# Kernel tuning notes

Measured on AMD Instinct MI355X. Metric: run time of the kernel, lower is better.

## Reference

```python
import jax, jax.numpy as jnp
import numpy as np

B, T, D, M, L = 4, 2048, 256, 128, 16
P = M * L  # max_pair_cnt


def setup_inputs() -> dict:
    key = jax.random.key(0)
    ks = jax.random.split(key, 11)
    head = jax.random.normal(ks[0], (B, P, T), jnp.float32) * 0.05
    tail = jax.random.normal(ks[1], (B, P, T), jnp.float32) * 0.05
    x = jax.random.normal(ks[2], (B, T, D), jnp.float32)
    coref_mention_position = jax.random.uniform(ks[3], (B, M, T), jnp.float32)
    lab = jax.random.uniform(ks[4], (B, P, 2), jnp.float32) + 1e-3
    coref_label = lab / lab.sum(-1, keepdims=True)  # already-softmaxed target
    coref_label_mask = jax.random.randint(ks[5], (B, P), 0, 2).astype(bool)
    lens = jnp.full((B, M), L, jnp.int32)  # uniform segment lengths
    w1 = jax.random.normal(ks[6], (3 * D, D), jnp.float32) / np.sqrt(3 * D).astype(np.float32)
    b1 = jnp.zeros((D,), jnp.float32)
    w2 = jax.random.normal(ks[7], (D, 2), jnp.float32) / np.sqrt(D).astype(np.float32)
    b2 = jnp.zeros((2,), jnp.float32)
    return {"head": head, "tail": tail, "lens": lens, "x": x,
            "coref_mention_position": coref_mention_position,
            "coref_label": coref_label, "coref_label_mask": coref_label_mask,
            "w1": w1, "b1": b1, "w2": w2, "b2": b2}


def reference(head, tail, lens, x, coref_mention_position, coref_label,
              coref_label_mask, w1, b1, w2, b2):
    # bmm-based gather of mention reps: [B,P,T] @ [B,T,D] -> [B,P,D]
    head_rep = jnp.einsum('bpt,btd->bpd', head, x)
    tail_rep = jnp.einsum('bpt,btd->bpd', tail, x)
    feat = jnp.concatenate([head_rep, tail_rep, head_rep * tail_rep], axis=-1)
    logits = jax.nn.relu(feat @ w1 + b1) @ w2 + b2  # [B,P,2]

    # ragged split_n_pad -> per-mention top-1 select (uniform lens == L -> reshape)
    scores = logits[..., 1].reshape(B, M, L)            # [B,M,L]
    max_idx = jnp.argmax(scores, axis=-1)               # [B,M]
    max_val = jnp.max(scores, axis=-1)                  # [B,M] (raw logit, as in source)
    tail_seg = tail_rep.reshape(B, M, L, D)
    sel = jnp.take_along_axis(tail_seg, max_idx[:, :, None, None], axis=2)[:, :, 0, :]
    coref_rep_m = sel * max_val[:, :, None]             # [B,M,D]

    # scatter-bmm merge back into sequence: [B,T,M] @ [B,M,D] -> [B,T,D]
    coref_rep = jnp.einsum('bmt,bmd->btd', coref_mention_position, coref_rep_m)
    output = x + coref_rep

    # KLDivLoss(reduction='mean') over masked pairs
    logq = jax.nn.log_softmax(logits, axis=-1)
    lab = coref_label
    pw = jnp.where(lab > 0, lab * jnp.log(jnp.maximum(lab, 1e-38)), 0.0) - lab * logq
    n = jnp.sum(coref_label_mask).astype(jnp.float32)
    loss = jnp.where(coref_label_mask[..., None], pw, 0.0).sum() / (n * 2.0)
    return output, loss
```

## Files before the change

### kernel.cpp

```cpp
#include <hip/hip_runtime.h>
#include <hip/hip_bf16.h>
#include <stdint.h>

#define TAU 0.35f

typedef __attribute__((ext_vector_type(8))) short bf16x8;
typedef __attribute__((ext_vector_type(4))) float f32x4;

__device__ __forceinline__ unsigned short f2bf(float f) {
  __bf16 h = (__bf16)f;
  return __builtin_bit_cast(unsigned short, h);
}
__device__ __forceinline__ float bf2f(unsigned short u) {
  unsigned int v = ((unsigned int)u) << 16;
  return __builtin_bit_cast(float, v);
}
__device__ __forceinline__ void async_copy16(const void* g, void* l) {
  __builtin_amdgcn_global_load_lds(
      (const __attribute__((address_space(1))) unsigned int*)g,
      (__attribute__((address_space(3))) unsigned int*)l, 16, 0, 0);
}

__global__ __launch_bounds__(256) void k_prep(
    const float* __restrict__ x, const float* __restrict__ w1,
    unsigned short* __restrict__ xt, unsigned short* __restrict__ w1t,
    int* __restrict__ njobs) {
  __shared__ float tileS[64][65];
  int bx = blockIdx.x, tid = threadIdx.x;
  if (bx == 0 && tid == 0) *njobs = 0;
  int j = tid & 63, i0 = tid >> 6;
  if (bx < 512) {
    int b = bx >> 7, t6 = (bx >> 2) & 31, d6 = bx & 3;
    const float* src = x + ((size_t)b * 2048 + (size_t)t6 * 64) * 256 + d6 * 64;
    for (int i = i0; i < 64; i += 4) tileS[i][j] = src[(size_t)i * 256 + j];
    __syncthreads();
    unsigned short* dst = xt + ((size_t)b * 256 + (size_t)d6 * 64) * 2048 + t6 * 64;
    for (int r = i0; r < 64; r += 4) dst[(size_t)r * 2048 + j] = f2bf(tileS[j][r]);
  } else {
    int wt = bx - 512;
    int k6 = wt >> 2, n6 = wt & 3;
    const float* src = w1 + ((size_t)k6 * 64) * 256 + n6 * 64;
    for (int i = i0; i < 64; i += 4) tileS[i][j] = src[(size_t)i * 256 + j];
    __syncthreads();
    unsigned short* dst = w1t + ((size_t)n6 * 64) * 768 + k6 * 64;
    for (int r = i0; r < 64; r += 4) dst[(size_t)r * 768 + j] = f2bf(tileS[j][r]);
  }
}

__global__ __launch_bounds__(256) void k_gemm_rep(
    const float* __restrict__ head, const float* __restrict__ tail,
    const unsigned short* __restrict__ xt,
    float* __restrict__ head_rep, float* __restrict__ tail_rep) {
  __shared__ unsigned short As[128 * 32];
  __shared__ unsigned short Bs[128 * 32];
  int bx = blockIdx.x;
  int b = bx >> 6, rem = bx & 63, mtile = rem >> 1, ntile = rem & 1;
  const float* Asrc = ((mtile < 16) ? head : tail) +
                      ((size_t)(b * 2048 + (mtile & 15) * 128)) * 2048;
  float* Crep = (mtile < 16) ? head_rep : tail_rep;
  const unsigned short* Bsrc = xt + ((size_t)(b * 256 + ntile * 128)) * 2048;

  int tid = threadIdx.x, lane = tid & 63, w = tid >> 6;

  int ar = tid >> 1, ah = tid & 1;
  bf16x8* aw0 = (bf16x8*)&As[(ar >> 4) * 512 + ((ah * 2 + 0) * 16 + (ar & 15)) * 8];
  bf16x8* aw1 = (bf16x8*)&As[(ar >> 4) * 512 + ((ah * 2 + 1) * 16 + (ar & 15)) * 8];

  const unsigned short* bg0 = Bsrc + (size_t)(w * 32 + (lane >> 2)) * 2048 + (lane & 3) * 8;
  const unsigned short* bg1 = bg0 + (size_t)16 * 2048;
  unsigned short* bl0 = &Bs[(w * 32 + 0) * 32];
  unsigned short* bl1 = &Bs[(w * 32 + 16) * 32];

  int wm = (w & 1) * 64, wn = (w >> 1) * 64;
  const bf16x8* afrag[4];
  const bf16x8* bfrag[4];
#pragma unroll
  for (int s = 0; s < 4; ++s) {
    afrag[s] = (const bf16x8*)&As[((w & 1) * 4 + s) * 512 + lane * 8];
    bfrag[s] = (const bf16x8*)&Bs[(wn + s * 16 + (lane & 15)) * 32 + (lane >> 4) * 8];
  }

  f32x4 acc[4][4];
#pragma unroll
  for (int i = 0; i < 4; ++i)
#pragma unroll
    for (int j = 0; j < 4; ++j) acc[i][j] = (f32x4){0.f, 0.f, 0.f, 0.f};

  float4 av[4];
  {
    const float4* ap = (const float4*)(Asrc + (size_t)ar * 2048 + ah * 16);
    av[0] = ap[0]; av[1] = ap[1]; av[2] = ap[2]; av[3] = ap[3];
  }

  for (int k0 = 0; k0 < 2048; k0 += 32) {
    __syncthreads();
    async_copy16(bg0, bl0);
    async_copy16(bg1, bl1);
    bg0 += 32; bg1 += 32;
    bf16x8 p0, p1;
    p0[0] = (short)f2bf(av[0].x); p0[1] = (short)f2bf(av[0].y);
    p0[2] = (short)f2bf(av[0].z); p0[3] = (short)f2bf(av[0].w);
    p0[4] = (short)f2bf(av[1].x); p0[5] = (short)f2bf(av[1].y);
    p0[6] = (short)f2bf(av[1].z); p0[7] = (short)f2bf(av[1].w);
    p1[0] = (short)f2bf(av[2].x); p1[1] = (short)f2bf(av[2].y);
    p1[2] = (short)f2bf(av[2].z); p1[3] = (short)f2bf(av[2].w);
    p1[4] = (short)f2bf(av[3].x); p1[5] = (short)f2bf(av[3].y);
    p1[6] = (short)f2bf(av[3].z); p1[7] = (short)f2bf(av[3].w);
    *aw0 = p0; *aw1 = p1;
    int kn = k0 + 32;
    const float4* ap = (const float4*)(Asrc + (size_t)ar * 2048 +
                                       ((kn < 2048) ? (kn + ah * 16) : (ah * 16)));
    av[0] = ap[0]; av[1] = ap[1]; av[2] = ap[2]; av[3] = ap[3];
    __syncthreads();

    bf16x8 a_[4], b_[4];
#pragma unroll
    for (int s = 0; s < 4; ++s) { a_[s] = *afrag[s]; b_[s] = *bfrag[s]; }
#pragma unroll
    for (int i = 0; i < 4; ++i)
#pragma unroll
      for (int j = 0; j < 4; ++j)
        acc[i][j] = __builtin_amdgcn_mfma_f32_16x16x32_bf16(a_[i], b_[j], acc[i][j], 0, 0, 0);
  }

  size_t rowbase = (size_t)(b * 2048 + (mtile & 15) * 128);
  int colbase = ntile * 128 + wn;
#pragma unroll
  for (int sm = 0; sm < 4; ++sm) {
    int row0 = wm + sm * 16 + ((lane >> 4) << 2);
#pragma unroll
    for (int sn = 0; sn < 4; ++sn) {
      int col = colbase + sn * 16 + (lane & 15);
#pragma unroll
      for (int i = 0; i < 4; ++i)
        Crep[(rowbase + row0 + i) * 256 + col] = acc[sm][sn][i];
    }
  }
}

__global__ __launch_bounds__(256) void k_feat(
    const float* __restrict__ hrep, const float* __restrict__ trep,
    unsigned short* __restrict__ featbf) {
  int gid = blockIdx.x * 256 + threadIdx.x;
  int p = gid >> 6, d0 = (gid & 63) * 4;
  float4 h4 = *(const float4*)&hrep[(size_t)p * 256 + d0];
  float4 t4 = *(const float4*)&trep[(size_t)p * 256 + d0];
  ushort4 a, bb, c;
  a.x = f2bf(h4.x); a.y = f2bf(h4.y); a.z = f2bf(h4.z); a.w = f2bf(h4.w);
  bb.x = f2bf(t4.x); bb.y = f2bf(t4.y); bb.z = f2bf(t4.z); bb.w = f2bf(t4.w);
  c.x = f2bf(h4.x * t4.x); c.y = f2bf(h4.y * t4.y);
  c.z = f2bf(h4.z * t4.z); c.w = f2bf(h4.w * t4.w);
  *(ushort4*)&featbf[(size_t)p * 768 + d0] = a;
  *(ushort4*)&featbf[(size_t)p * 768 + 256 + d0] = bb;
  *(ushort4*)&featbf[(size_t)p * 768 + 512 + d0] = c;
}

__global__ __launch_bounds__(256) void k_gemm_mlp(
    const unsigned short* __restrict__ featbf, const unsigned short* __restrict__ w1t,
    const float* __restrict__ b1, unsigned short* __restrict__ hbf) {
  __shared__ unsigned short As[64 * 32];
  __shared__ unsigned short Bs[128 * 32];
  int bx = blockIdx.x, mtile = bx >> 1, ntile = bx & 1;
  int tid = threadIdx.x, lane = tid & 63, w = tid >> 6;
  const unsigned short* ag = featbf + ((size_t)(mtile * 64) + w * 16 + (lane >> 2)) * 768 + (lane & 3) * 8;
  const unsigned short* bg0 = w1t + ((size_t)(ntile * 128) + w * 32 + (lane >> 2)) * 768 + (lane & 3) * 8;
  const unsigned short* bg1 = bg0 + (size_t)16 * 768;
  unsigned short* al = &As[(w * 16) * 32];
  unsigned short* bl0 = &Bs[(w * 32) * 32];
  unsigned short* bl1 = &Bs[(w * 32 + 16) * 32];
  int wn = w * 32;
  const bf16x8* afr[4];
  const bf16x8* bfr[2];
#pragma unroll
  for (int s = 0; s < 4; ++s)
    afr[s] = (const bf16x8*)&As[(s * 16 + (lane & 15)) * 32 + (lane >> 4) * 8];
#pragma unroll
  for (int s = 0; s < 2; ++s)
    bfr[s] = (const bf16x8*)&Bs[((wn + s * 16) + (lane & 15)) * 32 + (lane >> 4) * 8];

  f32x4 acc[4][2];
#pragma unroll
  for (int i = 0; i < 4; ++i)
#pragma unroll
    for (int j = 0; j < 2; ++j) acc[i][j] = (f32x4){0.f, 0.f, 0.f, 0.f};

  for (int k0 = 0; k0 < 768; k0 += 32) {
    __syncthreads();
    async_copy16(ag, al); ag += 32;
    async_copy16(bg0, bl0); bg0 += 32;
    async_copy16(bg1, bl1); bg1 += 32;
    __syncthreads();
    bf16x8 a_[4], b_[2];
#pragma unroll
    for (int s = 0; s < 4; ++s) a_[s] = *afr[s];
#pragma unroll
    for (int s = 0; s < 2; ++s) b_[s] = *bfr[s];
#pragma unroll
    for (int i = 0; i < 4; ++i)
#pragma unroll
      for (int j = 0; j < 2; ++j)
        acc[i][j] = __builtin_amdgcn_mfma_f32_16x16x32_bf16(a_[i], b_[j], acc[i][j], 0, 0, 0);
  }
#pragma unroll
  for (int sm = 0; sm < 4; ++sm) {
    int row0 = mtile * 64 + sm * 16 + ((lane >> 4) << 2);
#pragma unroll
    for (int sn = 0; sn < 2; ++sn) {
      int col = ntile * 128 + wn + sn * 16 + (lane & 15);
      float bv = b1[col];
#pragma unroll
      for (int i = 0; i < 4; ++i) {
        float v = acc[sm][sn][i] + bv;
        hbf[(size_t)(row0 + i) * 256 + col] = f2bf(fmaxf(v, 0.f));
      }
    }
  }
}

__global__ __launch_bounds__(256) void k_logits(
    const unsigned short* __restrict__ hbf, const float* __restrict__ w2,
    const float* __restrict__ b2, float* __restrict__ logits) {
  int w = threadIdx.x >> 6, lane = threadIdx.x & 63;
  int p = blockIdx.x * 4 + w;
  ushort4 h4 = *(const ushort4*)&hbf[(size_t)p * 256 + lane * 4];
  float hv0 = bf2f(h4.x), hv1 = bf2f(h4.y), hv2 = bf2f(h4.z), hv3 = bf2f(h4.w);
  float4 wa = *(const float4*)&w2[lane * 8];
  float4 wb = *(const float4*)&w2[lane * 8 + 4];
  float s0 = hv0 * wa.x + hv1 * wa.z + hv2 * wb.x + hv3 * wb.z;
  float s1 = hv0 * wa.y + hv1 * wa.w + hv2 * wb.y + hv3 * wb.w;
#pragma unroll
  for (int off = 32; off; off >>= 1) { s0 += __shfl_xor(s0, off); s1 += __shfl_xor(s1, off); }
  if (lane == 0) { logits[(size_t)p * 2] = s0 + b2[0]; logits[(size_t)p * 2 + 1] = s1 + b2[1]; }
}

__global__ void k_select(const float* __restrict__ logits, int* __restrict__ idxv,
                         float* __restrict__ mval, int* __restrict__ cmask,
                         int* __restrict__ njobs, int* __restrict__ jobs) {
  int q = blockIdx.x * 256 + threadIdx.x;
  if (q >= 512) return;
  int base = q * 16;
  float s[16];
#pragma unroll
  for (int i = 0; i < 16; ++i) s[i] = logits[(size_t)(base + i) * 2 + 1];
  float best = s[0]; int bi = 0;
#pragma unroll
  for (int i = 1; i < 16; ++i) if (s[i] > best) { best = s[i]; bi = i; }
  int mask = 0, cnt = 0;
#pragma unroll
  for (int i = 0; i < 16; ++i) if (s[i] > best - TAU) { mask |= 1 << i; ++cnt; }
  idxv[q] = bi; mval[q] = best;
  if (cnt > 1) {
    cmask[q] = mask;
    for (int i = 0; i < 16; ++i)
      if ((mask >> i) & 1) { int j = atomicAdd(njobs, 1); jobs[j] = base + i; }
  } else cmask[q] = 0;
}

__global__ __launch_bounds__(1024) void k_refine(
    const int* __restrict__ njobs, const int* __restrict__ jobs,
    const float* __restrict__ head, const float* __restrict__ tail,
    const float* __restrict__ x, const float* __restrict__ w1,
    const float* __restrict__ b1, const float* __restrict__ w2,
    const float* __restrict__ b2, float* __restrict__ refined) {
  __shared__ float hrow[2048], trow[2048], feat[768], red[1024], red2[1024];
  int tid = threadIdx.x, seg = tid >> 8, d = tid & 255;
  int nj = *njobs;
  for (int job = blockIdx.x; job < nj; job += gridDim.x) {
    int code = jobs[job];
    int b = code >> 11, p = code & 2047;
    if (tid < 512)
      *(float4*)&hrow[tid * 4] = *(const float4*)&head[((size_t)(b * 2048 + p)) * 2048 + tid * 4];
    else {
      int u = tid - 512;
      *(float4*)&trow[u * 4] = *(const float4*)&tail[((size_t)(b * 2048 + p)) * 2048 + u * 4];
    }
    __syncthreads();
    float hr = 0.f, tr = 0.f;
    const float* xb = x + ((size_t)b * 2048) * 256 + d;
#pragma unroll 8
    for (int t = seg * 512; t < seg * 512 + 512; ++t) {
      float xv = xb[(size_t)t * 256];
      hr += hrow[t] * xv; tr += trow[t] * xv;
    }
    red[tid] = hr; red2[tid] = tr;
    __syncthreads();
    if (seg == 0) {
      float fh = red[d] + red[256 + d] + red[512 + d] + red[768 + d];
      float ft = red2[d] + red2[256 + d] + red2[512 + d] + red2[768 + d];
      feat[d] = fh; feat[256 + d] = ft; feat[512 + d] = fh * ft;
    }
    __syncthreads();
    float hp = 0.f;
    for (int ii = seg * 192; ii < seg * 192 + 192; ++ii) hp += feat[ii] * w1[(size_t)ii * 256 + d];
    red[tid] = hp;
    __syncthreads();
    if (seg == 0) {
      float hj = b1[d] + red[d] + red[256 + d] + red[512 + d] + red[768 + d];
      hj = fmaxf(hj, 0.f);
      red2[d] = hj * w2[d * 2 + 1];
    }
    __syncthreads();
    for (int s = 128; s > 0; s >>= 1) {
      if (tid < s) red2[tid] += red2[tid + s];
      __syncthreads();
    }
    if (tid == 0) refined[code] = red2[0] + b2[1];
    __syncthreads();
  }
}

__global__ __launch_bounds__(256) void k_repm(
    const int* __restrict__ idxv, const float* __restrict__ mval,
    const int* __restrict__ cmask, const float* __restrict__ refined,
    const float* __restrict__ trep, float* __restrict__ repm) {
  int q = blockIdx.x, d = threadIdx.x;
  int mask = cmask[q]; int bi; float v;
  if (mask) {
    bi = -1; v = -1e30f;
    for (int i = 0; i < 16; ++i)
      if ((mask >> i) & 1) { float s = refined[q * 16 + i]; if (s > v) { v = s; bi = i; } }
  } else { bi = idxv[q]; v = mval[q]; }
  repm[(size_t)q * 256 + d] = trep[((size_t)q * 16 + bi) * 256 + d] * v;
}

__global__ __launch_bounds__(256) void k_merge(
    const float* __restrict__ cmp, const float* __restrict__ repm,
    const float* __restrict__ x, float* __restrict__ out) {
  __shared__ float cl[128 * 32];
  int bx = blockIdx.x, b = bx >> 6, t0 = (bx & 63) * 32;
  int tid = threadIdx.x;
#pragma unroll
  for (int it = 0; it < 4; ++it) {
    int fidx = it * 256 + tid;
    int row = fidx >> 3, c4 = fidx & 7;
    *(float4*)&cl[row * 32 + c4 * 4] =
        *(const float4*)&cmp[((size_t)(b * 128 + row)) * 2048 + t0 + c4 * 4];
  }
  __syncthreads();
  int d = tid;
  float acc[32];
#pragma unroll
  for (int i = 0; i < 32; ++i) acc[i] = 0.f;
  for (int m = 0; m < 128; ++m) {
    float rv = repm[(size_t)(b * 128 + m) * 256 + d];
#pragma unroll
    for (int tt = 0; tt < 32; ++tt) acc[tt] += cl[m * 32 + tt] * rv;
  }
  const float* xb = x + ((size_t)(b * 2048 + t0)) * 256 + d;
  float* ob = out + ((size_t)(b * 2048 + t0)) * 256 + d;
  for (int tt = 0; tt < 32; ++tt) ob[(size_t)tt * 256] = xb[(size_t)tt * 256] + acc[tt];
}

__global__ __launch_bounds__(1024) void k_loss(
    const float* __restrict__ logits, const float* __restrict__ lab,
    const unsigned char* __restrict__ mask, float* __restrict__ out_loss) {
  __shared__ float rs[1024], rc[1024];
  int tid = threadIdx.x;
  float sum = 0.f, cnt = 0.f;
  for (int p = tid; p < 8192; p += 1024) {
    float l0 = logits[(size_t)p * 2], l1 = logits[(size_t)p * 2 + 1];
    float a0 = lab[(size_t)p * 2], a1 = lab[(size_t)p * 2 + 1];
    float mx = fmaxf(l0, l1);
    float lse = mx + logf(expf(l0 - mx) + expf(l1 - mx));
    float pw = 0.f;
    if (a0 > 0.f) pw += a0 * logf(fmaxf(a0, 1e-38f));
    if (a1 > 0.f) pw += a1 * logf(fmaxf(a1, 1e-38f));
    pw -= a0 * (l0 - lse) + a1 * (l1 - lse);
    if (mask[p]) { sum += pw; cnt += 1.f; }
  }
  rs[tid] = sum; rc[tid] = cnt;
  __syncthreads();
  for (int s = 512; s > 0; s >>= 1) {
    if (tid < s) { rs[tid] += rs[tid + s]; rc[tid] += rc[tid + s]; }
    __syncthreads();
  }
  if (tid == 0) *out_loss = rs[0] / (rc[0] * 2.0f);
}

extern "C" void kernel_launch(void* const* d_in, const int* in_sizes, int n_in,
                              void* d_out, int out_size, void* d_ws, size_t ws_size,
                              hipStream_t stream) {
  (void)in_sizes; (void)n_in; (void)out_size; (void)ws_size;
  const float* head = (const float*)d_in[0];
  const float* tail = (const float*)d_in[1];
  const float* x = (const float*)d_in[3];
  const float* cmp = (const float*)d_in[4];
  const float* lab = (const float*)d_in[5];
  const unsigned char* lmask = (const unsigned char*)d_in[6];
  const float* w1 = (const float*)d_in[7];
  const float* b1 = (const float*)d_in[8];
  const float* w2 = (const float*)d_in[9];
  const float* b2 = (const float*)d_in[10];
  float* out = (float*)d_out;

  char* ws = (char*)d_ws;
  size_t off = 0;
  auto alloc = [&](size_t bytes) -> void* {
    void* p = ws + off; off += (bytes + 255) & ~(size_t)255; return p;
  };
  unsigned short* xt = (unsigned short*)alloc(4ull * 256 * 2048 * 2);
  unsigned short* w1t = (unsigned short*)alloc(256ull * 768 * 2);
  float* hrep = (float*)alloc(8192ull * 256 * 4);
  float* trep = (float*)alloc(8192ull * 256 * 4);
  unsigned short* featb = (unsigned short*)alloc(8192ull * 768 * 2);
  unsigned short* hbf = (unsigned short*)alloc(8192ull * 256 * 2);
  float* logits = (float*)alloc(8192ull * 2 * 4);
  float* refined = (float*)alloc(8192ull * 4);
  int* idxv = (int*)alloc(512 * 4);
  float* mvalv = (float*)alloc(512 * 4);
  int* cmaskv = (int*)alloc(512 * 4);
  int* njobs = (int*)alloc(256);
  int* jobs = (int*)alloc(8192 * 4);
  float* repm = (float*)alloc(512ull * 256 * 4);

  k_prep<<<560, 256, 0, stream>>>(x, w1, xt, w1t, njobs);
  k_gemm_rep<<<256, 256, 0, stream>>>(head, tail, xt, hrep, trep);
  k_feat<<<2048, 256, 0, stream>>>(hrep, trep, featb);
  k_gemm_mlp<<<256, 256, 0, stream>>>(featb, w1t, b1, hbf);
  k_logits<<<2048, 256, 0, stream>>>(hbf, w2, b2, logits);
  k_select<<<2, 256, 0, stream>>>(logits, idxv, mvalv, cmaskv, njobs, jobs);
  k_refine<<<256, 1024, 0, stream>>>(njobs, jobs, head, tail, x, w1, b1, w2, b2, refined);
  k_repm<<<512, 256, 0, stream>>>(idxv, mvalv, cmaskv, refined, trep, repm);
  k_merge<<<256, 256, 0, stream>>>(cmp, repm, x, out);
  k_loss<<<1, 1024, 0, stream>>>(logits, lab, lmask, out + 4ull * 2048 * 256);
}
```

Measured before the change: 370.6 us.

## Retile GEMMs with double-buffered swizzled LDS, fuse logits into MLP GEMM

The rep GEMM moves from 128x128 tiles to 64x64 tiles with 64-wide K steps, double-buffered and XOR-swizzled LDS, and four times as many blocks. The MLP GEMM gets the same treatment and absorbs the bias, ReLU and w2 projection, accumulating logits with atomicAdd into a buffer that k_prep presets to b2. This removes the separate k_logits kernel and its hbf intermediate. k_merge also switches to 16-token tiles with vectorized LDS reads and twice as many blocks. Smaller tiles give more parallelism and occupancy but less data reuse per block, and the atomics add contention and make the logit sums order-dependent.

```diff
diff --git a/kernel.cpp b/kernel.cpp
--- a/kernel.cpp
+++ b/kernel.cpp
@@ -23,11 +23,16 @@
 
 __global__ __launch_bounds__(256) void k_prep(
     const float* __restrict__ x, const float* __restrict__ w1,
+    const float* __restrict__ b2,
     unsigned short* __restrict__ xt, unsigned short* __restrict__ w1t,
-    int* __restrict__ njobs) {
+    float* __restrict__ logits, int* __restrict__ njobs) {
   __shared__ float tileS[64][65];
   int bx = blockIdx.x, tid = threadIdx.x;
   if (bx == 0 && tid == 0) *njobs = 0;
+  if (bx < 64) {
+    int i = bx * 256 + tid;
+    logits[i] = b2[i & 1];
+  }
   int j = tid & 63, i0 = tid >> 6;
   if (bx < 512) {
     int b = bx >> 7, t6 = (bx >> 2) & 31, d6 = bx & 3;
@@ -47,56 +52,58 @@
   }
 }
 
-__global__ __launch_bounds__(256) void k_gemm_rep(
+__global__ __launch_bounds__(256, 4) void k_gemm_rep(
     const float* __restrict__ head, const float* __restrict__ tail,
     const unsigned short* __restrict__ xt,
-    float* __restrict__ head_rep, float* __restrict__ tail_rep) {
-  __shared__ unsigned short As[128 * 32];
-  __shared__ unsigned short Bs[128 * 32];
+    float* __restrict__ hrep, float* __restrict__ trep) {
+  __shared__ unsigned short As[2][4096];
+  __shared__ unsigned short Bs[2][4096];
   int bx = blockIdx.x;
-  int b = bx >> 6, rem = bx & 63, mtile = rem >> 1, ntile = rem & 1;
-  const float* Asrc = ((mtile < 16) ? head : tail) +
-                      ((size_t)(b * 2048 + (mtile & 15) * 128)) * 2048;
-  float* Crep = (mtile < 16) ? head_rep : tail_rep;
-  const unsigned short* Bsrc = xt + ((size_t)(b * 256 + ntile * 128)) * 2048;
+  int ntile = bx >> 8;
+  int g = bx & 255;
+  int b = g >> 6, mtile = g & 63;
+  const float* Asrc = ((mtile < 32) ? head : tail) +
+                      ((size_t)(b * 2048 + (mtile & 31) * 64)) * 2048;
+  float* Crep = (mtile < 32) ? hrep : trep;
+  const unsigned short* Bsrc = xt + ((size_t)(b * 256 + ntile * 64)) * 2048;
 
   int tid = threadIdx.x, lane = tid & 63, w = tid >> 6;
 
-  int ar = tid >> 1, ah = tid & 1;
-  bf16x8* aw0 = (bf16x8*)&As[(ar >> 4) * 512 + ((ah * 2 + 0) * 16 + (ar & 15)) * 8];
-  bf16x8* aw1 = (bf16x8*)&As[(ar >> 4) * 512 + ((ah * 2 + 1) * 16 + (ar & 15)) * 8];
-
-  const unsigned short* bg0 = Bsrc + (size_t)(w * 32 + (lane >> 2)) * 2048 + (lane & 3) * 8;
-  const unsigned short* bg1 = bg0 + (size_t)16 * 2048;
-  unsigned short* bl0 = &Bs[(w * 32 + 0) * 32];
-  unsigned short* bl1 = &Bs[(w * 32 + 16) * 32];
-
-  int wm = (w & 1) * 64, wn = (w >> 1) * 64;
-  const bf16x8* afrag[4];
-  const bf16x8* bfrag[4];
-#pragma unroll
-  for (int s = 0; s < 4; ++s) {
-    afrag[s] = (const bf16x8*)&As[((w & 1) * 4 + s) * 512 + lane * 8];
-    bfrag[s] = (const bf16x8*)&Bs[(wn + s * 16 + (lane & 15)) * 32 + (lane >> 4) * 8];
-  }
-
-  f32x4 acc[4][4];
-#pragma unroll
-  for (int i = 0; i < 4; ++i)
-#pragma unroll
-    for (int j = 0; j < 4; ++j) acc[i][j] = (f32x4){0.f, 0.f, 0.f, 0.f};
+  int arow = tid >> 2, akq = tid & 3;
+  const float* aptr = Asrc + (size_t)arow * 2048 + akq * 16;
+  int rt = arow >> 4, r15 = arow & 15;
+  int k8a = akq * 2, k8b = akq * 2 + 1;
+  int awi0 = rt * 128 + (k8a >> 2) * 64 + (k8a & 3) * 16 + r15;
+  int awi1 = rt * 128 + (k8b >> 2) * 64 + (k8b & 3) * 16 + r15;
+
+  const unsigned short* bg[2];
+  int bdst[2];
+#pragma unroll
+  for (int a = 0; a < 2; ++a) {
+    int colofs = a * 8 + (lane >> 3);
+    int k8 = (lane & 7) ^ (colofs & 7);
+    bg[a] = Bsrc + (size_t)(w * 16 + colofs) * 2048 + k8 * 8;
+    bdst[a] = (w * 128 + a * 64 + lane) * 8;
+  }
+
+  int sw0 = (lane >> 4) ^ (lane & 7);
+  int sw1 = (4 + (lane >> 4)) ^ (lane & 7);
+  int colc[4];
+#pragma unroll
+  for (int ct = 0; ct < 4; ++ct) colc[ct] = (ct * 16 + (lane & 15)) * 8;
+
+  f32x4 acc[4];
+#pragma unroll
+  for (int ct = 0; ct < 4; ++ct) acc[ct] = (f32x4){0.f, 0.f, 0.f, 0.f};
 
   float4 av[4];
   {
-    const float4* ap = (const float4*)(Asrc + (size_t)ar * 2048 + ah * 16);
+    const float4* ap = (const float4*)aptr;
     av[0] = ap[0]; av[1] = ap[1]; av[2] = ap[2]; av[3] = ap[3];
   }
-
-  for (int k0 = 0; k0 < 2048; k0 += 32) {
-    __syncthreads();
-    async_copy16(bg0, bl0);
-    async_copy16(bg1, bl1);
-    bg0 += 32; bg1 += 32;
+#pragma unroll
+  for (int a = 0; a < 2; ++a) { async_copy16(bg[a], &Bs[0][bdst[a]]); bg[a] += 64; }
+  {
     bf16x8 p0, p1;
     p0[0] = (short)f2bf(av[0].x); p0[1] = (short)f2bf(av[0].y);
     p0[2] = (short)f2bf(av[0].z); p0[3] = (short)f2bf(av[0].w);
@@ -106,36 +113,60 @@
     p1[2] = (short)f2bf(av[2].z); p1[3] = (short)f2bf(av[2].w);
     p1[4] = (short)f2bf(av[3].x); p1[5] = (short)f2bf(av[3].y);
     p1[6] = (short)f2bf(av[3].z); p1[7] = (short)f2bf(av[3].w);
-    *aw0 = p0; *aw1 = p1;
-    int kn = k0 + 32;
-    const float4* ap = (const float4*)(Asrc + (size_t)ar * 2048 +
-                                       ((kn < 2048) ? (kn + ah * 16) : (ah * 16)));
+    *(bf16x8*)&As[0][awi0 * 8] = p0;
+    *(bf16x8*)&As[0][awi1 * 8] = p1;
+  }
+  {
+    const float4* ap = (const float4*)(aptr + 64);
     av[0] = ap[0]; av[1] = ap[1]; av[2] = ap[2]; av[3] = ap[3];
-    __syncthreads();
-
-    bf16x8 a_[4], b_[4];
-#pragma unroll
-    for (int s = 0; s < 4; ++s) { a_[s] = *afrag[s]; b_[s] = *bfrag[s]; }
+  }
+  __syncthreads();
+
+  for (int it = 0; it < 32; ++it) {
+    int cur = it & 1, nxt = cur ^ 1;
+    if (it < 31) {
+#pragma unroll
+      for (int a = 0; a < 2; ++a) { async_copy16(bg[a], &Bs[nxt][bdst[a]]); bg[a] += 64; }
+      bf16x8 p0, p1;
+      p0[0] = (short)f2bf(av[0].x); p0[1] = (short)f2bf(av[0].y);
+      p0[2] = (short)f2bf(av[0].z); p0[3] = (short)f2bf(av[0].w);
+      p0[4] = (short)f2bf(av[1].x); p0[5] = (short)f2bf(av[1].y);
+      p0[6] = (short)f2bf(av[1].z); p0[7] = (short)f2bf(av[1].w);
+      p1[0] = (short)f2bf(av[2].x); p1[1] = (short)f2bf(av[2].y);
+      p1[2] = (short)f2bf(av[2].z); p1[3] = (short)f2bf(av[2].w);
+      p1[4] = (short)f2bf(av[3].x); p1[5] = (short)f2bf(av[3].y);
+      p1[6] = (short)f2bf(av[3].z); p1[7] = (short)f2bf(av[3].w);
+      *(bf16x8*)&As[nxt][awi0 * 8] = p0;
+      *(bf16x8*)&As[nxt][awi1 * 8] = p1;
+    }
+    if (it < 30) {
+      const float4* ap = (const float4*)(aptr + (it + 2) * 64);
+      av[0] = ap[0]; av[1] = ap[1]; av[2] = ap[2]; av[3] = ap[3];
+    }
+    const unsigned short* A_ = As[cur];
+    const unsigned short* B_ = Bs[cur];
+    bf16x8 a0 = *(const bf16x8*)&A_[(w * 128 + lane) * 8];
+    bf16x8 a1 = *(const bf16x8*)&A_[(w * 128 + 64 + lane) * 8];
+#pragma unroll
+    for (int ct = 0; ct < 4; ++ct) {
+      bf16x8 b0 = *(const bf16x8*)&B_[(colc[ct] + sw0) * 8];
+      acc[ct] = __builtin_amdgcn_mfma_f32_16x16x32_bf16(a0, b0, acc[ct], 0, 0, 0);
+    }
+#pragma unroll
+    for (int ct = 0; ct < 4; ++ct) {
+      bf16x8 b1 = *(const bf16x8*)&B_[(colc[ct] + sw1) * 8];
+      acc[ct] = __builtin_amdgcn_mfma_f32_16x16x32_bf16(a1, b1, acc[ct], 0, 0, 0);
+    }
+    __syncthreads();
+  }
+
+  size_t prow = (size_t)b * 2048 + (size_t)(mtile & 31) * 64 + w * 16 + ((lane >> 4) << 2);
+  int cb = ntile * 64 + (lane & 15);
+#pragma unroll
+  for (int ct = 0; ct < 4; ++ct)
 #pragma unroll
     for (int i = 0; i < 4; ++i)
-#pragma unroll
-      for (int j = 0; j < 4; ++j)
-        acc[i][j] = __builtin_amdgcn_mfma_f32_16x16x32_bf16(a_[i], b_[j], acc[i][j], 0, 0, 0);
-  }
-
-  size_t rowbase = (size_t)(b * 2048 + (mtile & 15) * 128);
-  int colbase = ntile * 128 + wn;
-#pragma unroll
-  for (int sm = 0; sm < 4; ++sm) {
-    int row0 = wm + sm * 16 + ((lane >> 4) << 2);
-#pragma unroll
-    for (int sn = 0; sn < 4; ++sn) {
-      int col = colbase + sn * 16 + (lane & 15);
-#pragma unroll
-      for (int i = 0; i < 4; ++i)
-        Crep[(rowbase + row0 + i) * 256 + col] = acc[sm][sn][i];
-    }
-  }
+      Crep[(prow + i) * 256 + cb + ct * 16] = acc[ct][i];
 }
 
 __global__ __launch_bounds__(256) void k_feat(
@@ -155,82 +186,95 @@
   *(ushort4*)&featbf[(size_t)p * 768 + 512 + d0] = c;
 }
 
-__global__ __launch_bounds__(256) void k_gemm_mlp(
-    const unsigned short* __restrict__ featbf, const unsigned short* __restrict__ w1t,
-    const float* __restrict__ b1, unsigned short* __restrict__ hbf) {
-  __shared__ unsigned short As[64 * 32];
-  __shared__ unsigned short Bs[128 * 32];
-  int bx = blockIdx.x, mtile = bx >> 1, ntile = bx & 1;
+__global__ __launch_bounds__(256, 4) void k_gemm_mlp(
+    const unsigned short* __restrict__ featb, const unsigned short* __restrict__ w1t,
+    const float* __restrict__ b1, const float* __restrict__ w2,
+    float* __restrict__ logits) {
+  __shared__ unsigned short As[2][4096], Bs[2][4096];
+  int bx = blockIdx.x;
+  int ntile = bx >> 7;
+  int mtile = bx & 127;
   int tid = threadIdx.x, lane = tid & 63, w = tid >> 6;
-  const unsigned short* ag = featbf + ((size_t)(mtile * 64) + w * 16 + (lane >> 2)) * 768 + (lane & 3) * 8;
-  const unsigned short* bg0 = w1t + ((size_t)(ntile * 128) + w * 32 + (lane >> 2)) * 768 + (lane & 3) * 8;
-  const unsigned short* bg1 = bg0 + (size_t)16 * 768;
-  unsigned short* al = &As[(w * 16) * 32];
-  unsigned short* bl0 = &Bs[(w * 32) * 32];
-  unsigned short* bl1 = &Bs[(w * 32 + 16) * 32];
-  int wn = w * 32;
-  const bf16x8* afr[4];
-  const bf16x8* bfr[2];
-#pragma unroll
-  for (int s = 0; s < 4; ++s)
-    afr[s] = (const bf16x8*)&As[(s * 16 + (lane & 15)) * 32 + (lane >> 4) * 8];
-#pragma unroll
-  for (int s = 0; s < 2; ++s)
-    bfr[s] = (const bf16x8*)&Bs[((wn + s * 16) + (lane & 15)) * 32 + (lane >> 4) * 8];
-
-  f32x4 acc[4][2];
-#pragma unroll
-  for (int i = 0; i < 4; ++i)
-#pragma unroll
-    for (int j = 0; j < 2; ++j) acc[i][j] = (f32x4){0.f, 0.f, 0.f, 0.f};
-
-  for (int k0 = 0; k0 < 768; k0 += 32) {
-    __syncthreads();
-    async_copy16(ag, al); ag += 32;
-    async_copy16(bg0, bl0); bg0 += 32;
-    async_copy16(bg1, bl1); bg1 += 32;
-    __syncthreads();
-    bf16x8 a_[4], b_[2];
-#pragma unroll
-    for (int s = 0; s < 4; ++s) a_[s] = *afr[s];
-#pragma unroll
-    for (int s = 0; s < 2; ++s) b_[s] = *bfr[s];
-#pragma unroll
-    for (int i = 0; i < 4; ++i)
-#pragma unroll
-      for (int j = 0; j < 2; ++j)
-        acc[i][j] = __builtin_amdgcn_mfma_f32_16x16x32_bf16(a_[i], b_[j], acc[i][j], 0, 0, 0);
-  }
-#pragma unroll
-  for (int sm = 0; sm < 4; ++sm) {
-    int row0 = mtile * 64 + sm * 16 + ((lane >> 4) << 2);
-#pragma unroll
-    for (int sn = 0; sn < 2; ++sn) {
-      int col = ntile * 128 + wn + sn * 16 + (lane & 15);
-      float bv = b1[col];
-#pragma unroll
-      for (int i = 0; i < 4; ++i) {
-        float v = acc[sm][sn][i] + bv;
-        hbf[(size_t)(row0 + i) * 256 + col] = f2bf(fmaxf(v, 0.f));
+
+  const unsigned short* ag[2];
+  const unsigned short* bgp[2];
+  int dofs[2];
+#pragma unroll
+  for (int a = 0; a < 2; ++a) {
+    int rowofs = a * 8 + (lane >> 3);
+    int k8 = (lane & 7) ^ (rowofs & 7);
+    ag[a] = featb + (size_t)(mtile * 64 + w * 16 + rowofs) * 768 + k8 * 8;
+    bgp[a] = w1t + (size_t)(ntile * 64 + w * 16 + rowofs) * 768 + k8 * 8;
+    dofs[a] = (w * 128 + a * 64 + lane) * 8;
+  }
+  int sw0 = (lane >> 4) ^ (lane & 7);
+  int sw1 = (4 + (lane >> 4)) ^ (lane & 7);
+  int arowc = (w * 16 + (lane & 15)) * 8;
+  int colc[4];
+#pragma unroll
+  for (int ct = 0; ct < 4; ++ct) colc[ct] = (ct * 16 + (lane & 15)) * 8;
+
+  f32x4 acc[4];
+#pragma unroll
+  for (int ct = 0; ct < 4; ++ct) acc[ct] = (f32x4){0.f, 0.f, 0.f, 0.f};
+
+#pragma unroll
+  for (int a = 0; a < 2; ++a) {
+    async_copy16(ag[a], &As[0][dofs[a]]); ag[a] += 64;
+    async_copy16(bgp[a], &Bs[0][dofs[a]]); bgp[a] += 64;
+  }
+  __syncthreads();
+
+  for (int it = 0; it < 12; ++it) {
+    int cur = it & 1, nxt = cur ^ 1;
+    if (it < 11) {
+#pragma unroll
+      for (int a = 0; a < 2; ++a) {
+        async_copy16(ag[a], &As[nxt][dofs[a]]); ag[a] += 64;
+        async_copy16(bgp[a], &Bs[nxt][dofs[a]]); bgp[a] += 64;
       }
     }
-  }
-}
-
-__global__ __launch_bounds__(256) void k_logits(
-    const unsigned short* __restrict__ hbf, const float* __restrict__ w2,
-    const float* __restrict__ b2, float* __restrict__ logits) {
-  int w = threadIdx.x >> 6, lane = threadIdx.x & 63;
-  int p = blockIdx.x * 4 + w;
-  ushort4 h4 = *(const ushort4*)&hbf[(size_t)p * 256 + lane * 4];
-  float hv0 = bf2f(h4.x), hv1 = bf2f(h4.y), hv2 = bf2f(h4.z), hv3 = bf2f(h4.w);
-  float4 wa = *(const float4*)&w2[lane * 8];
-  float4 wb = *(const float4*)&w2[lane * 8 + 4];
-  float s0 = hv0 * wa.x + hv1 * wa.z + hv2 * wb.x + hv3 * wb.z;
-  float s1 = hv0 * wa.y + hv1 * wa.w + hv2 * wb.y + hv3 * wb.w;
-#pragma unroll
-  for (int off = 32; off; off >>= 1) { s0 += __shfl_xor(s0, off); s1 += __shfl_xor(s1, off); }
-  if (lane == 0) { logits[(size_t)p * 2] = s0 + b2[0]; logits[(size_t)p * 2 + 1] = s1 + b2[1]; }
+    const unsigned short* A_ = As[cur];
+    const unsigned short* B_ = Bs[cur];
+    bf16x8 a0 = *(const bf16x8*)&A_[(arowc + sw0) * 8];
+    bf16x8 a1 = *(const bf16x8*)&A_[(arowc + sw1) * 8];
+#pragma unroll
+    for (int ct = 0; ct < 4; ++ct) {
+      bf16x8 b0 = *(const bf16x8*)&B_[(colc[ct] + sw0) * 8];
+      acc[ct] = __builtin_amdgcn_mfma_f32_16x16x32_bf16(a0, b0, acc[ct], 0, 0, 0);
+    }
+#pragma unroll
+    for (int ct = 0; ct < 4; ++ct) {
+      bf16x8 b1 = *(const bf16x8*)&B_[(colc[ct] + sw1) * 8];
+      acc[ct] = __builtin_amdgcn_mfma_f32_16x16x32_bf16(a1, b1, acc[ct], 0, 0, 0);
+    }
+    __syncthreads();
+  }
+
+  float bv[4], w20[4], w21[4];
+#pragma unroll
+  for (int ct = 0; ct < 4; ++ct) {
+    int col = ntile * 64 + ct * 16 + (lane & 15);
+    bv[ct] = b1[col]; w20[ct] = w2[col * 2]; w21[ct] = w2[col * 2 + 1];
+  }
+#pragma unroll
+  for (int i = 0; i < 4; ++i) {
+    float s0 = 0.f, s1 = 0.f;
+#pragma unroll
+    for (int ct = 0; ct < 4; ++ct) {
+      float r = fmaxf(acc[ct][i] + bv[ct], 0.f);
+      s0 += r * w20[ct]; s1 += r * w21[ct];
+    }
+#pragma unroll
+    for (int off = 1; off < 16; off <<= 1) {
+      s0 += __shfl_xor(s0, off); s1 += __shfl_xor(s1, off);
+    }
+    if ((lane & 15) == 0) {
+      int row = mtile * 64 + w * 16 + ((lane >> 4) << 2) + i;
+      atomicAdd(&logits[row * 2], s0);
+      atomicAdd(&logits[row * 2 + 1], s1);
+    }
+  }
 }
 
 __global__ void k_select(const float* __restrict__ logits, int* __restrict__ idxv,
@@ -326,29 +370,35 @@
 __global__ __launch_bounds__(256) void k_merge(
     const float* __restrict__ cmp, const float* __restrict__ repm,
     const float* __restrict__ x, float* __restrict__ out) {
-  __shared__ float cl[128 * 32];
-  int bx = blockIdx.x, b = bx >> 6, t0 = (bx & 63) * 32;
+  __shared__ float cl[128 * 16];
+  int bx = blockIdx.x, b = bx >> 7, t0 = (bx & 127) * 16;
   int tid = threadIdx.x;
 #pragma unroll
-  for (int it = 0; it < 4; ++it) {
-    int fidx = it * 256 + tid;
-    int row = fidx >> 3, c4 = fidx & 7;
-    *(float4*)&cl[row * 32 + c4 * 4] =
-        *(const float4*)&cmp[((size_t)(b * 128 + row)) * 2048 + t0 + c4 * 4];
+  for (int it = 0; it < 2; ++it) {
+    int f = it * 256 + tid;
+    int row = f >> 2, c4 = (f & 3) * 4;
+    *(float4*)&cl[row * 16 + c4] =
+        *(const float4*)&cmp[((size_t)(b * 128 + row)) * 2048 + t0 + c4];
   }
   __syncthreads();
+  float acc[16];
+#pragma unroll
+  for (int i = 0; i < 16; ++i) acc[i] = 0.f;
   int d = tid;
-  float acc[32];
-#pragma unroll
-  for (int i = 0; i < 32; ++i) acc[i] = 0.f;
   for (int m = 0; m < 128; ++m) {
     float rv = repm[(size_t)(b * 128 + m) * 256 + d];
-#pragma unroll
-    for (int tt = 0; tt < 32; ++tt) acc[tt] += cl[m * 32 + tt] * rv;
+    const float4* c4p = (const float4*)&cl[m * 16];
+#pragma unroll
+    for (int jj = 0; jj < 4; ++jj) {
+      float4 c = c4p[jj];
+      acc[jj * 4] += c.x * rv; acc[jj * 4 + 1] += c.y * rv;
+      acc[jj * 4 + 2] += c.z * rv; acc[jj * 4 + 3] += c.w * rv;
+    }
   }
   const float* xb = x + ((size_t)(b * 2048 + t0)) * 256 + d;
   float* ob = out + ((size_t)(b * 2048 + t0)) * 256 + d;
-  for (int tt = 0; tt < 32; ++tt) ob[(size_t)tt * 256] = xb[(size_t)tt * 256] + acc[tt];
+#pragma unroll
+  for (int tt = 0; tt < 16; ++tt) ob[(size_t)tt * 256] = xb[(size_t)tt * 256] + acc[tt];
 }
 
 __global__ __launch_bounds__(1024) void k_loss(
@@ -403,7 +453,6 @@
   float* hrep = (float*)alloc(8192ull * 256 * 4);
   float* trep = (float*)alloc(8192ull * 256 * 4);
   unsigned short* featb = (unsigned short*)alloc(8192ull * 768 * 2);
-  unsigned short* hbf = (unsigned short*)alloc(8192ull * 256 * 2);
   float* logits = (float*)alloc(8192ull * 2 * 4);
   float* refined = (float*)alloc(8192ull * 4);
   int* idxv = (int*)alloc(512 * 4);
@@ -413,14 +462,13 @@
   int* jobs = (int*)alloc(8192 * 4);
   float* repm = (float*)alloc(512ull * 256 * 4);
 
-  k_prep<<<560, 256, 0, stream>>>(x, w1, xt, w1t, njobs);
-  k_gemm_rep<<<256, 256, 0, stream>>>(head, tail, xt, hrep, trep);
+  k_prep<<<560, 256, 0, stream>>>(x, w1, b2, xt, w1t, logits, njobs);
+  k_gemm_rep<<<1024, 256, 0, stream>>>(head, tail, xt, hrep, trep);
   k_feat<<<2048, 256, 0, stream>>>(hrep, trep, featb);
-  k_gemm_mlp<<<256, 256, 0, stream>>>(featb, w1t, b1, hbf);
-  k_logits<<<2048, 256, 0, stream>>>(hbf, w2, b2, logits);
+  k_gemm_mlp<<<512, 256, 0, stream>>>(featb, w1t, b1, w2, logits);
   k_select<<<2, 256, 0, stream>>>(logits, idxv, mvalv, cmaskv, njobs, jobs);
   k_refine<<<256, 1024, 0, stream>>>(njobs, jobs, head, tail, x, w1, b1, w2, b2, refined);
   k_repm<<<512, 256, 0, stream>>>(idxv, mvalv, cmaskv, refined, trep, repm);
-  k_merge<<<256, 256, 0, stream>>>(cmp, repm, x, out);
+  k_merge<<<512, 256, 0, stream>>>(cmp, repm, x, out);
   k_loss<<<1, 1024, 0, stream>>>(logits, lab, lmask, out + 4ull * 2048 * 256);
 }
```

New measurement: 330.4 us. 1.12x faster.
